# Kernel optimization log

Hardware: AMD Instinct MI355X
Metric: run time of the kernel (lower is better)

The kernel has to match this reference:

```python
import jax, jax.numpy as jnp
import numpy as np
from jax import lax

B, L, V, EMB = 256, 256, 14, 512
K = 16  # LSH bits (capped so 2**k fits int32)


def _conv2d(x, w, b):
    # x: [B,C,H,W], w: [O,I,3,3], padding=1 -> SAME
    y = lax.conv_general_dilated(x, w, (1, 1), ((1, 1), (1, 1)),
                                 dimension_numbers=("NCHW", "OIHW", "NCHW"))
    return y + b[None, :, None, None]


def _maxpool1d(x):  # [B,C,L] -> [B,C,L//2], kernel=stride=2
    b, c, l = x.shape
    return x.reshape(b, c, l // 2, 2).max(-1)


def _branch(tokens, emb, cw, cb, lw, lb):
    # Embedding -> pool over sequence -> Conv2d(3x3,pad1) on [C, L//2, 1] -> Linear
    e = emb[tokens]                     # [B,L,512]
    e = jnp.transpose(e, (0, 2, 1))     # [B,512,L]
    e = _maxpool1d(e)[..., None]        # [B,512,L//2,1]
    e = _conv2d(e, cw, cb)              # [B,256,L//2,1]
    return e.reshape(e.shape[0], -1) @ lw + lb


def _fog_of_war(enemy_out, rand_proj):
    # lsh_hash: random projection -> sign bits -> integer representation
    bits = (enemy_out @ rand_proj > 0).astype(jnp.int32)          # [B,K]
    pow2 = 2 ** jnp.arange(K - 1, -1, -1, dtype=jnp.int32)
    integer_repr = (bits * pow2).sum(axis=1)                      # [B] (computed as in original; loop doesn't read it)
    n = integer_repr.shape[0]
    # Greedy loop: remainder starts as arange(n); all counts are 1, so argmax
    # picks the first remaining index each iteration, which is then removed.
    def step(mask, _):
        idx = jnp.argmax(mask)  # first True = smallest remaining index
        return mask.at[idx].set(False), idx
    _, order = lax.scan(step, jnp.ones((n,), jnp.bool_), None, length=n)
    return order  # == arange(n), the original's deterministic result


def setup_inputs() -> dict:
    key = jax.random.key(0)
    ks = jax.random.split(key, 18)
    s = 0.02
    return {
        "x": jax.random.randint(ks[0], (B, L), 0, V, dtype=jnp.int32),
        "enemy_emb": jax.random.normal(ks[1], (V, EMB), jnp.float32) * s,
        "enemy_conv_w": jax.random.normal(ks[2], (256, 512, 3, 3), jnp.float32) * s,
        "enemy_conv_b": jax.random.normal(ks[3], (256,), jnp.float32) * s,
        "enemy_lin_w": jax.random.normal(ks[4], (256 * (L // 2), 128), jnp.float32) * s,
        "enemy_lin_b": jax.random.normal(ks[5], (128,), jnp.float32) * s,
        "rand_proj": jax.random.normal(ks[6], (128, K), jnp.float32),
        "manip_conv_w": jax.random.normal(ks[7], (64, 128, 3, 3), jnp.float32) * s,
        "manip_conv_b": jax.random.normal(ks[8], (64,), jnp.float32) * s,
        "manip_lin_w": jax.random.normal(ks[9], (64 * (L // 2), 256), jnp.float32) * s,
        "manip_lin_b": jax.random.normal(ks[10], (256,), jnp.float32) * s,
        "friend_emb": jax.random.normal(ks[11], (V, EMB), jnp.float32) * s,
        "friend_conv_w": jax.random.normal(ks[12], (256, 512, 3, 3), jnp.float32) * s,
        "friend_conv_b": jax.random.normal(ks[13], (256,), jnp.float32) * s,
        "friend_lin1_w": jax.random.normal(ks[14], (256 * (L // 2), 128), jnp.float32) * s,
        "friend_lin1_b": jax.random.normal(ks[15], (128,), jnp.float32) * s,
        "friend_lin2_w": jax.random.normal(ks[16], (128, V), jnp.float32) * s,
        "friend_lin2_b": jax.random.normal(ks[17], (V,), jnp.float32) * s,
    }


def reference(x, enemy_emb, enemy_conv_w, enemy_conv_b, enemy_lin_w, enemy_lin_b,
              rand_proj, manip_conv_w, manip_conv_b, manip_lin_w, manip_lin_b,
              friend_emb, friend_conv_w, friend_conv_b, friend_lin1_w, friend_lin1_b,
              friend_lin2_w, friend_lin2_b):
    # enemy branch
    enemy_out = jax.nn.softmax(
        _branch(x, enemy_emb, enemy_conv_w, enemy_conv_b, enemy_lin_w, enemy_lin_b), axis=1)  # [B,128]
    # fog_of_war: LSH hash + greedy set-cover loop -> index order
    perm = _fog_of_war(enemy_out, rand_proj)  # [B] int
    # probability manipulator: Conv2d(128,64) expects [B,128,L//2,1]
    m_in = jnp.broadcast_to(enemy_out[perm][:, :, None, None], (B, 128, L // 2, 1))
    m = jax.nn.relu(_conv2d(m_in, manip_conv_w, manip_conv_b))   # [B,64,L//2,1]
    m = m.reshape(B, -1) @ manip_lin_w + manip_lin_b             # [B,256]
    # friend branch consumes manipulator output as a token sequence (Embedding needs ints)
    tokens = (jnp.floor(jnp.abs(m) * 100.0) % V).astype(jnp.int32)  # [B,256]
    f = _branch(tokens, friend_emb, friend_conv_w, friend_conv_b, friend_lin1_w, friend_lin1_b)
    f = f @ friend_lin2_w + friend_lin2_b                        # [B,14]
    return jax.nn.softmax(f, axis=1)
```

## Files before the change

kernel.cpp:

```cpp
#include <hip/hip_runtime.h>
#include <hip/hip_bf16.h>
#include <math.h>

#define BB    256
#define LL    256
#define NV    14
#define EMBD  512
#define H2    128
#define OC    256
#define NP    196
#define JD    128
#define MO    64
#define MJ    256

#define CB_MAIN   294
#define CB_MANIPW 48
#define CB_LINT   32

using s16x8 = __attribute__((ext_vector_type(8))) short;
using f32x4 = __attribute__((ext_vector_type(4))) float;

static __device__ __forceinline__ unsigned pk2(float a, float b) {
    union { __hip_bfloat162 h; unsigned u; } c;
    c.h = __float22bfloat162_rn(make_float2(a, b));
    return c.u;
}
static __device__ __forceinline__ void hilo2(float y0, float y1,
                                             unsigned &hi, unsigned &lo) {
    hi = pk2(y0, y1);
    float h0 = __uint_as_float(hi << 16);
    float h1 = __uint_as_float(hi & 0xFFFF0000u);
    lo = pk2(y0 - h0, y1 - h1);
}

__global__ void k_prep(const float* __restrict__ cw_e, const float* __restrict__ cw_f,
                       float* __restrict__ cwT) {
    __shared__ float T[48][66];
    int bid = blockIdx.x;
    int t = threadIdx.x;
    int ic = bid & 31;
    int oc = (bid >> 5) & 3;
    int br = bid >> 7;
    int i0 = ic * 16, o0 = oc * 64;
    const float* cw = br ? cw_f : cw_e;
    int ol = t >> 2, part = t & 3;
    const float* src = cw + ((size_t)(o0 + ol) * EMBD + i0) * 9 + part * 36;
    #pragma unroll
    for (int ii = 0; ii < 4; ++ii)
        #pragma unroll
        for (int kh = 0; kh < 3; ++kh)
            T[kh * 16 + part * 4 + ii][ol] = src[ii * 9 + kh * 3 + 1];
    __syncthreads();
    int lane = t & 63, r0 = t >> 6;
    for (int rr = r0; rr < 48; rr += 4) {
        int kh = rr >> 4, il = rr & 15;
        cwT[(((size_t)(br * 3 + kh)) * EMBD + i0 + il) * OC + o0 + lane] = T[rr][lane];
    }
}

__global__ __launch_bounds__(512) void k_contrib(
        const float* __restrict__ emb_e, const float* __restrict__ emb_f,
        const float* __restrict__ cwT,
        const float* __restrict__ cb_e, const float* __restrict__ cb_f,
        const float* __restrict__ mcw, const float* __restrict__ mlw,
        float* __restrict__ C, float* __restrict__ Wc, float* __restrict__ Lint) {
    int bid = blockIdx.x;
    int t = threadIdx.x;
    if (bid < CB_MAIN) {
        int qg = bid % 49;
        int kh = (bid / 49) % 3;
        int br = bid / 147;
        int o = t & 255, ih = t >> 8;
        const float* emb = br ? emb_f : emb_e;

        __shared__ float Pl[4][512];
        __shared__ float Rd[4][2][256];
        for (int idx = t; idx < 4 * 512; idx += 512) {
            int row = idx >> 9, col = idx & 511;
            int q = qg * 4 + row;
            int t1 = q / NV, t2 = q % NV;
            Pl[row][col] = fmaxf(emb[t1 * EMBD + col], emb[t2 * EMBD + col]);
        }
        __syncthreads();

        const float* w = cwT + ((size_t)(br * 3 + kh) * EMBD + ih * 256) * OC + o;
        float acc[4] = {0.f, 0.f, 0.f, 0.f};
        #pragma unroll 8
        for (int i = 0; i < 256; i++) {
            float wv = w[(size_t)i * OC];
            #pragma unroll
            for (int qq = 0; qq < 4; qq++) acc[qq] = fmaf(wv, Pl[qq][ih * 256 + i], acc[qq]);
        }
        #pragma unroll
        for (int qq = 0; qq < 4; qq++) Rd[qq][ih][o] = acc[qq];
        __syncthreads();
        if (t < 256) {
            float cbv = (kh == 1) ? (br ? cb_f[o] : cb_e[o]) : 0.f;
            #pragma unroll
            for (int qq = 0; qq < 4; qq++)
                C[(((size_t)br * NP + qg * 4 + qq) * 3 + kh) * OC + o] =
                    Rd[qq][0][o] + Rd[qq][1][o] + cbv;
        }
    } else if (bid < CB_MAIN + CB_MANIPW) {
        int idx = (bid - CB_MAIN) * 512 + t;
        int o = idx & 63;
        int i = (idx >> 6) & 127;
        int cls = idx >> 13;
        const float* base = mcw + ((size_t)(o * 128 + i) * 3) * 3 + 1;
        float v = 0.f;
        if (cls != 2) { v += base[3]; v += base[6]; }
        else          { v += base[0]; v += base[3]; }
        if (cls == 1)   v += base[0];
        Wc[idx] = v;
    } else {
        int lb = bid - (CB_MAIN + CB_MANIPW);
        int o = lb * 2 + (t >> 8);
        int j = t & 255;
        float s = 0.f;
        for (int h = 1; h <= 126; h++)
            s += mlw[((size_t)(o * H2 + h)) * MJ + j];
        Lint[o * 256 + j] = s;
    }
}

template <int X3, int SK>
__global__ __launch_bounds__(512) void k_gemm(
        const int* __restrict__ tok, const float* __restrict__ C,
        const float* __restrict__ lw, float* __restrict__ partial) {
    __shared__ unsigned short Ah[2][64][SK + 4];
    __shared__ unsigned short Al[X3 ? 2 : 1][X3 ? 64 : 1][X3 ? SK + 4 : 1];
    __shared__ unsigned short Bh[2][128][SK + 4];
    __shared__ unsigned short Bl[X3 ? 2 : 1][X3 ? 128 : 1][X3 ? SK + 4 : 1];

    const int h  = blockIdx.x;
    const int B0 = blockIdx.y * 64;
    const int t  = threadIdx.x;
    constexpr int NST = 256 / SK;
    constexpr int KQ  = SK / 8;
    constexpr int KPT = SK / 16;

    const int am = t >> 3;
    const int kq = (t & 7) * KQ;
    const int* tb = tok + (size_t)(B0 + am) * LL;
    const int q1 = tb[2 * h] * NV + tb[2 * h + 1];
    const float* r1 = C + ((size_t)q1 * 3 + 1) * OC + kq;
    const float* r0 = nullptr;
    const float* r2 = nullptr;
    if (h > 0)      { int q0 = tb[2 * h - 2] * NV + tb[2 * h - 1]; r0 = C + ((size_t)q0 * 3 + 0) * OC + kq; }
    if (h < H2 - 1) { int q2 = tb[2 * h + 2] * NV + tb[2 * h + 3]; r2 = C + ((size_t)q2 * 3 + 2) * OC + kq; }

    const int j0b = (t & 31) * 4;
    const int k0  = (t >> 5) * KPT;
    const float* wsrc = lw + (((size_t)k0 * H2) + h) * JD + j0b;

    float4 ya[SK / 32], yb[SK / 32], yc[SK / 32], wv4[KPT];

    auto load = [&](int s) {
        #pragma unroll
        for (int p = 0; p < SK / 32; ++p) {
            ya[p] = *(const float4*)(r1 + s * SK + 4 * p);
            if (r0) yb[p] = *(const float4*)(r0 + s * SK + 4 * p);
            else    yb[p] = make_float4(0, 0, 0, 0);
            if (r2) yc[p] = *(const float4*)(r2 + s * SK + 4 * p);
            else    yc[p] = make_float4(0, 0, 0, 0);
        }
        #pragma unroll
        for (int kk = 0; kk < KPT; ++kk)
            wv4[kk] = *(const float4*)(wsrc + ((size_t)(s * SK) + kk) * (H2 * JD));
    };

    auto store = [&](int buf) {
        #pragma unroll
        for (int p = 0; p < SK / 32; ++p) {
            float y[4];
            y[0] = ya[p].x + yb[p].x + yc[p].x; y[1] = ya[p].y + yb[p].y + yc[p].y;
            y[2] = ya[p].z + yb[p].z + yc[p].z; y[3] = ya[p].w + yb[p].w + yc[p].w;
            if (X3) {
                unsigned h0, h1, l0, l1;
                hilo2(y[0], y[1], h0, l0);
                hilo2(y[2], y[3], h1, l1);
                *(uint2*)&Ah[buf][am][kq + 4 * p] = make_uint2(h0, h1);
                *(uint2*)&Al[buf][am][kq + 4 * p] = make_uint2(l0, l1);
            } else {
                *(uint2*)&Ah[buf][am][kq + 4 * p] =
                    make_uint2(pk2(y[0], y[1]), pk2(y[2], y[3]));
            }
        }
        #pragma unroll
        for (int jj = 0; jj < 4; ++jj) {
            float wf[KPT];
            #pragma unroll
            for (int kk = 0; kk < KPT; ++kk)
                wf[kk] = ((const float*)&wv4[kk])[jj];
            if constexpr (KPT == 2) {
                if (X3) {
                    unsigned hu, lu;
                    hilo2(wf[0], wf[1], hu, lu);
                    *(unsigned*)&Bh[buf][j0b + jj][k0] = hu;
                    *(unsigned*)&Bl[buf][j0b + jj][k0] = lu;
                } else {
                    *(unsigned*)&Bh[buf][j0b + jj][k0] = pk2(wf[0], wf[1]);
                }
            } else {
                if (X3) {
                    unsigned h0, h1, l0, l1;
                    hilo2(wf[0], wf[1], h0, l0);
                    hilo2(wf[2], wf[3], h1, l1);
                    *(uint2*)&Bh[buf][j0b + jj][k0] = make_uint2(h0, h1);
                    *(uint2*)&Bl[buf][j0b + jj][k0] = make_uint2(l0, l1);
                } else {
                    *(uint2*)&Bh[buf][j0b + jj][k0] =
                        make_uint2(pk2(wf[0], wf[1]), pk2(wf[2], wf[3]));
                }
            }
        }
    };

    const int lane = t & 63, wid = t >> 6;
    const int Wm = (wid >> 2) * 32;
    const int Wn = (wid & 3) * 32;
    const int fr = lane & 15;
    const int g8 = (lane >> 4) * 8;

    f32x4 acc[2][2] = {};

    auto rd8 = [&](const unsigned short* p) -> s16x8 {
        union { s16x8 v; uint2 u[2]; } tmp;
        tmp.u[0] = *(const uint2*)(p);
        tmp.u[1] = *(const uint2*)(p + 4);
        return tmp.v;
    };

    auto compute = [&](int buf) {
        #pragma unroll
        for (int kk0 = 0; kk0 < SK; kk0 += 32) {
            s16x8 a_h[2], b_h[2];
            #pragma unroll
            for (int mf = 0; mf < 2; ++mf) a_h[mf] = rd8(&Ah[buf][Wm + mf * 16 + fr][kk0 + g8]);
            #pragma unroll
            for (int nf = 0; nf < 2; ++nf) b_h[nf] = rd8(&Bh[buf][Wn + nf * 16 + fr][kk0 + g8]);
            #pragma unroll
            for (int mf = 0; mf < 2; ++mf)
                #pragma unroll
                for (int nf = 0; nf < 2; ++nf)
                    acc[mf][nf] = __builtin_amdgcn_mfma_f32_16x16x32_bf16(a_h[mf], b_h[nf], acc[mf][nf], 0, 0, 0);
            if (X3) {
                s16x8 a_l[2], b_l[2];
                #pragma unroll
                for (int mf = 0; mf < 2; ++mf) a_l[mf] = rd8(&Al[buf][Wm + mf * 16 + fr][kk0 + g8]);
                #pragma unroll
                for (int nf = 0; nf < 2; ++nf) b_l[nf] = rd8(&Bl[buf][Wn + nf * 16 + fr][kk0 + g8]);
                #pragma unroll
                for (int mf = 0; mf < 2; ++mf)
                    #pragma unroll
                    for (int nf = 0; nf < 2; ++nf) {
                        acc[mf][nf] = __builtin_amdgcn_mfma_f32_16x16x32_bf16(a_h[mf], b_l[nf], acc[mf][nf], 0, 0, 0);
                        acc[mf][nf] = __builtin_amdgcn_mfma_f32_16x16x32_bf16(a_l[mf], b_h[nf], acc[mf][nf], 0, 0, 0);
                    }
            }
        }
    };

    load(0);
    store(0);
    __syncthreads();
    for (int s = 0; s < NST; ++s) {
        if (s < NST - 1) load(s + 1);
        compute(s & 1);
        if (s < NST - 1) store((s + 1) & 1);
        __syncthreads();
    }

    float* pb = partial + (((size_t)(B0 + Wm)) * H2 + h) * JD + Wn;
    #pragma unroll
    for (int mf = 0; mf < 2; ++mf)
        #pragma unroll
        for (int nf = 0; nf < 2; ++nf)
            #pragma unroll
            for (int r = 0; r < 4; ++r) {
                int row = mf * 16 + (lane >> 4) * 4 + r;
                int col = nf * 16 + fr;
                pb[(size_t)row * H2 * JD + col] = acc[mf][nf][r];
            }
}

__global__ __launch_bounds__(512) void k_fuseE(
        const float* __restrict__ partial, const float* __restrict__ elb,
        const float* __restrict__ Wc, const float* __restrict__ mcb,
        const float* __restrict__ mlw, const float* __restrict__ Lint,
        const float* __restrict__ mlb, int* __restrict__ tokens) {
    int b = blockIdx.x, t = threadIdx.x;
    __shared__ float S[4][128];
    __shared__ float eo[128];
    __shared__ float m3[3][64];
    __shared__ float red[128];
    __shared__ float mt[2][256];

    int j = t & 127, hh = t >> 7;
    float s = 0.f;
    const float* pbase = partial + (size_t)b * H2 * JD + j;
    for (int h = hh * 32; h < hh * 32 + 32; ++h)
        s += pbase[(size_t)h * JD];
    S[hh][j] = s;
    __syncthreads();
    if (t < 128) {
        float v = (S[0][t] + S[1][t]) + (S[2][t] + S[3][t]) + elb[t];
        S[0][t] = v;
        red[t] = v;
    }
    __syncthreads();
    for (int st = 64; st > 0; st >>= 1) {
        if (t < st) red[t] = fmaxf(red[t], red[t + st]);
        __syncthreads();
    }
    float mx = red[0];
    __syncthreads();
    if (t < 128) {
        float e = expf(S[0][t] - mx);
        eo[t] = e;
        red[t] = e;
    }
    __syncthreads();
    for (int st = 64; st > 0; st >>= 1) {
        if (t < st) red[t] += red[t + st];
        __syncthreads();
    }
    float inv = 1.f / red[0];
    __syncthreads();
    if (t < 128) eo[t] *= inv;
    __syncthreads();
    if (t < 192) {
        int cls = t >> 6, o = t & 63;
        float a = mcb[o];
        const float* wp = Wc + (size_t)cls * 128 * 64 + o;
        for (int i = 0; i < 128; ++i) a = fmaf(eo[i], wp[(size_t)i * 64], a);
        m3[cls][o] = fmaxf(a, 0.f);
    }
    __syncthreads();
    {
        int ihh = t >> 8, jj = t & 255;
        float a = ihh ? 0.f : mlb[jj];
        for (int o = ihh * 32; o < ihh * 32 + 32; ++o) {
            a = fmaf(m3[0][o], mlw[((size_t)(o * H2 + 0)) * MJ + jj], a);
            a = fmaf(m3[1][o], Lint[(size_t)o * MJ + jj], a);
            a = fmaf(m3[2][o], mlw[((size_t)(o * H2 + 127)) * MJ + jj], a);
        }
        mt[ihh][jj] = a;
    }
    __syncthreads();
    if (t < 256) {
        float a = mt[0][t] + mt[1][t];
        tokens[(size_t)b * LL + t] = ((int)floorf(fabsf(a) * 100.f)) % NV;
    }
}

__global__ __launch_bounds__(512) void k_fuseF(
        const float* __restrict__ partial, const float* __restrict__ flb1,
        const float* __restrict__ fl2, const float* __restrict__ fb2,
        float* __restrict__ outp) {
    int b = blockIdx.x, t = threadIdx.x;
    __shared__ float S[4][128];
    __shared__ float f1[128];
    __shared__ float sl[NV];
    int j = t & 127, hh = t >> 7;
    float s = 0.f;
    const float* pbase = partial + (size_t)b * H2 * JD + j;
    for (int h = hh * 32; h < hh * 32 + 32; ++h)
        s += pbase[(size_t)h * JD];
    S[hh][j] = s;
    __syncthreads();
    if (t < 128) f1[t] = (S[0][t] + S[1][t]) + (S[2][t] + S[3][t]) + flb1[t];
    __syncthreads();
    if (t < NV) {
        float a = fb2[t];
        for (int jj = 0; jj < 128; ++jj) a = fmaf(f1[jj], fl2[(size_t)jj * NV + t], a);
        sl[t] = a;
    }
    __syncthreads();
    if (t < NV) {
        float mx = -1e30f;
        for (int u = 0; u < NV; ++u) mx = fmaxf(mx, sl[u]);
        float ss = 0.f;
        for (int u = 0; u < NV; ++u) ss += expf(sl[u] - mx);
        outp[(size_t)b * NV + t] = expf(sl[t] - mx) / ss;
    }
}

extern "C" void kernel_launch(void* const* d_in, const int* in_sizes, int n_in,
                              void* d_out, int out_size, void* d_ws, size_t ws_size,
                              hipStream_t stream) {
    const int*   x    = (const int*)d_in[0];
    const float* eemb = (const float*)d_in[1];
    const float* ecw  = (const float*)d_in[2];
    const float* ecb  = (const float*)d_in[3];
    const float* elw  = (const float*)d_in[4];
    const float* elb  = (const float*)d_in[5];
    const float* mcw  = (const float*)d_in[7];
    const float* mcb  = (const float*)d_in[8];
    const float* mlw  = (const float*)d_in[9];
    const float* mlb  = (const float*)d_in[10];
    const float* femb = (const float*)d_in[11];
    const float* fcw  = (const float*)d_in[12];
    const float* fcb  = (const float*)d_in[13];
    const float* flw1 = (const float*)d_in[14];
    const float* flb1 = (const float*)d_in[15];
    const float* fl2  = (const float*)d_in[16];
    const float* fb2  = (const float*)d_in[17];
    float* outp = (float*)d_out;

    char* w = (char*)d_ws;
    size_t off = 0;
    auto alloc = [&](size_t bytes) {
        void* p = w + off;
        off = (off + bytes + 255) & ~(size_t)255;
        return p;
    };
    float* cwT    = (float*)alloc(2ull * 3 * EMBD * OC * 4);
    float* C      = (float*)alloc(2ull * NP * 3 * OC * 4);
    float* Wc     = (float*)alloc(3ull * 128 * 64 * 4);
    float* Lint   = (float*)alloc(64ull * MJ * 4);
    int*   tokens = (int*)alloc((size_t)BB * LL * 4);
    float* partial= (float*)alloc((size_t)BB * H2 * JD * 4);

    const float* C_e = C;
    const float* C_f = C + (size_t)NP * 3 * OC;

    k_prep<<<256, 256, 0, stream>>>(ecw, fcw, cwT);
    k_contrib<<<CB_MAIN + CB_MANIPW + CB_LINT, 512, 0, stream>>>(
        eemb, femb, cwT, ecb, fcb, mcw, mlw, C, Wc, Lint);

    k_gemm<1, 32><<<dim3(H2, 4), 512, 0, stream>>>(x, C_e, elw, partial);
    k_fuseE<<<BB, 512, 0, stream>>>(partial, elb, Wc, mcb, mlw, Lint, mlb, tokens);

    k_gemm<0, 64><<<dim3(H2, 4), 512, 0, stream>>>(tokens, C_f, flw1, partial);
    k_fuseF<<<BB, 512, 0, stream>>>(partial, flb1, fl2, fb2, outp);
}
```

Baseline: 75.10 us.

## Retile per-position GEMM to 32-row blocks covering two sequence positions each

The per-position GEMM kernel now gives each block 32 batch rows instead of 64 and has it loop over two adjacent sequence positions, accumulating both into one partial result. The partial buffer is halved and the fuse kernels reduce over 64 position groups instead of 128. This halves the partial-sum traffic and the reduction work, keeping the block count at 512. In exchange each block runs twice as many pipeline stages with fewer MFMAs per wave per stage, so the weight tile loaded per stage is reused by half as many rows.

New measurement: 84.99 us. +13.2%, slower.

```diff
diff --git a/kernel.cpp b/kernel.cpp
--- a/kernel.cpp
+++ b/kernel.cpp
@@ -12,6 +12,7 @@
 #define JD    128
 #define MO    64
 #define MJ    256
+#define GH    64
 
 #define CB_MAIN   294
 #define CB_MANIPW 48
@@ -124,66 +125,93 @@
 }
 
 template <int X3, int SK>
-__global__ __launch_bounds__(512) void k_gemm(
+__global__ __launch_bounds__(512) void k_gemm32(
         const int* __restrict__ tok, const float* __restrict__ C,
         const float* __restrict__ lw, float* __restrict__ partial) {
-    __shared__ unsigned short Ah[2][64][SK + 4];
-    __shared__ unsigned short Al[X3 ? 2 : 1][X3 ? 64 : 1][X3 ? SK + 4 : 1];
+    constexpr int NST = 256 / SK;
+    constexpr int U   = 2 * NST;
+    constexpr int KA  = SK / 16;
+    constexpr int KPT = SK / 16;
+
+    __shared__ unsigned short Ah[2][32][SK + 4];
+    __shared__ unsigned short Al[X3 ? 2 : 1][X3 ? 32 : 1][X3 ? SK + 4 : 1];
     __shared__ unsigned short Bh[2][128][SK + 4];
     __shared__ unsigned short Bl[X3 ? 2 : 1][X3 ? 128 : 1][X3 ? SK + 4 : 1];
 
-    const int h  = blockIdx.x;
-    const int B0 = blockIdx.y * 64;
+    const int hg = blockIdx.x;
+    const int h0 = hg * 2;
+    const int B0 = blockIdx.y * 32;
     const int t  = threadIdx.x;
-    constexpr int NST = 256 / SK;
-    constexpr int KQ  = SK / 8;
-    constexpr int KPT = SK / 16;
-
-    const int am = t >> 3;
-    const int kq = (t & 7) * KQ;
+
+    const int am = t >> 4;
+    const int kq = (t & 15) * KA;
     const int* tb = tok + (size_t)(B0 + am) * LL;
-    const int q1 = tb[2 * h] * NV + tb[2 * h + 1];
-    const float* r1 = C + ((size_t)q1 * 3 + 1) * OC + kq;
-    const float* r0 = nullptr;
-    const float* r2 = nullptr;
-    if (h > 0)      { int q0 = tb[2 * h - 2] * NV + tb[2 * h - 1]; r0 = C + ((size_t)q0 * 3 + 0) * OC + kq; }
-    if (h < H2 - 1) { int q2 = tb[2 * h + 2] * NV + tb[2 * h + 3]; r2 = C + ((size_t)q2 * 3 + 2) * OC + kq; }
 
     const int j0b = (t & 31) * 4;
     const int k0  = (t >> 5) * KPT;
-    const float* wsrc = lw + (((size_t)k0 * H2) + h) * JD + j0b;
-
-    float4 ya[SK / 32], yb[SK / 32], yc[SK / 32], wv4[KPT];
+
+    const float *r1, *r0, *r2, *wsrc;
+    auto setptr = [&](int h) {
+        int q1 = tb[2 * h] * NV + tb[2 * h + 1];
+        r1 = C + ((size_t)q1 * 3 + 1) * OC + kq;
+        r0 = nullptr; r2 = nullptr;
+        if (h > 0)      { int q0 = tb[2 * h - 2] * NV + tb[2 * h - 1]; r0 = C + ((size_t)q0 * 3 + 0) * OC + kq; }
+        if (h < H2 - 1) { int q2 = tb[2 * h + 2] * NV + tb[2 * h + 3]; r2 = C + ((size_t)q2 * 3 + 2) * OC + kq; }
+        wsrc = lw + ((size_t)k0 * H2 + h) * JD + j0b;
+    };
+
+    float ya[KA], ybv[KA], ycv[KA];
+    float4 wv4[KPT];
+
+    auto ldv = [&](const float* p, float* d) {
+        if constexpr (KA == 2) {
+            float2 v = *(const float2*)p;
+            d[0] = v.x; d[1] = v.y;
+        } else {
+            float4 v = *(const float4*)p;
+            d[0] = v.x; d[1] = v.y; d[2] = v.z; d[3] = v.w;
+        }
+    };
 
     auto load = [&](int s) {
-        #pragma unroll
-        for (int p = 0; p < SK / 32; ++p) {
-            ya[p] = *(const float4*)(r1 + s * SK + 4 * p);
-            if (r0) yb[p] = *(const float4*)(r0 + s * SK + 4 * p);
-            else    yb[p] = make_float4(0, 0, 0, 0);
-            if (r2) yc[p] = *(const float4*)(r2 + s * SK + 4 * p);
-            else    yc[p] = make_float4(0, 0, 0, 0);
+        ldv(r1 + s * SK, ya);
+        if (r0) {
+            ldv(r0 + s * SK, ybv);
+        } else {
+            for (int e = 0; e < KA; ++e) ybv[e] = 0.f;
+        }
+        if (r2) {
+            ldv(r2 + s * SK, ycv);
+        } else {
+            for (int e = 0; e < KA; ++e) ycv[e] = 0.f;
         }
         #pragma unroll
         for (int kk = 0; kk < KPT; ++kk)
-            wv4[kk] = *(const float4*)(wsrc + ((size_t)(s * SK) + kk) * (H2 * JD));
+            wv4[kk] = *(const float4*)(wsrc + ((size_t)(s * SK + kk) * H2) * JD);
     };
 
     auto store = [&](int buf) {
-        #pragma unroll
-        for (int p = 0; p < SK / 32; ++p) {
-            float y[4];
-            y[0] = ya[p].x + yb[p].x + yc[p].x; y[1] = ya[p].y + yb[p].y + yc[p].y;
-            y[2] = ya[p].z + yb[p].z + yc[p].z; y[3] = ya[p].w + yb[p].w + yc[p].w;
+        float y[KA];
+        #pragma unroll
+        for (int e = 0; e < KA; ++e) y[e] = ya[e] + ybv[e] + ycv[e];
+        if constexpr (KA == 2) {
             if (X3) {
-                unsigned h0, h1, l0, l1;
-                hilo2(y[0], y[1], h0, l0);
-                hilo2(y[2], y[3], h1, l1);
-                *(uint2*)&Ah[buf][am][kq + 4 * p] = make_uint2(h0, h1);
-                *(uint2*)&Al[buf][am][kq + 4 * p] = make_uint2(l0, l1);
+                unsigned hu, lu;
+                hilo2(y[0], y[1], hu, lu);
+                *(unsigned*)&Ah[buf][am][kq] = hu;
+                *(unsigned*)&Al[buf][am][kq] = lu;
             } else {
-                *(uint2*)&Ah[buf][am][kq + 4 * p] =
-                    make_uint2(pk2(y[0], y[1]), pk2(y[2], y[3]));
+                *(unsigned*)&Ah[buf][am][kq] = pk2(y[0], y[1]);
+            }
+        } else {
+            if (X3) {
+                unsigned h0u, h1u, l0u, l1u;
+                hilo2(y[0], y[1], h0u, l0u);
+                hilo2(y[2], y[3], h1u, l1u);
+                *(uint2*)&Ah[buf][am][kq] = make_uint2(h0u, h1u);
+                *(uint2*)&Al[buf][am][kq] = make_uint2(l0u, l1u);
+            } else {
+                *(uint2*)&Ah[buf][am][kq] = make_uint2(pk2(y[0], y[1]), pk2(y[2], y[3]));
             }
         }
         #pragma unroll
@@ -203,11 +231,11 @@
                 }
             } else {
                 if (X3) {
-                    unsigned h0, h1, l0, l1;
-                    hilo2(wf[0], wf[1], h0, l0);
-                    hilo2(wf[2], wf[3], h1, l1);
-                    *(uint2*)&Bh[buf][j0b + jj][k0] = make_uint2(h0, h1);
-                    *(uint2*)&Bl[buf][j0b + jj][k0] = make_uint2(l0, l1);
+                    unsigned h0u, h1u, l0u, l1u;
+                    hilo2(wf[0], wf[1], h0u, l0u);
+                    hilo2(wf[2], wf[3], h1u, l1u);
+                    *(uint2*)&Bh[buf][j0b + jj][k0] = make_uint2(h0u, h1u);
+                    *(uint2*)&Bl[buf][j0b + jj][k0] = make_uint2(l0u, l1u);
                 } else {
                     *(uint2*)&Bh[buf][j0b + jj][k0] =
                         make_uint2(pk2(wf[0], wf[1]), pk2(wf[2], wf[3]));
@@ -217,12 +245,12 @@
     };
 
     const int lane = t & 63, wid = t >> 6;
-    const int Wm = (wid >> 2) * 32;
+    const int Wm = (wid >> 2) * 16;
     const int Wn = (wid & 3) * 32;
     const int fr = lane & 15;
     const int g8 = (lane >> 4) * 8;
 
-    f32x4 acc[2][2] = {};
+    f32x4 acc[2] = {};
 
     auto rd8 = [&](const unsigned short* p) -> s16x8 {
         union { s16x8 v; uint2 u[2]; } tmp;
@@ -234,54 +262,52 @@
     auto compute = [&](int buf) {
         #pragma unroll
         for (int kk0 = 0; kk0 < SK; kk0 += 32) {
-            s16x8 a_h[2], b_h[2];
-            #pragma unroll
-            for (int mf = 0; mf < 2; ++mf) a_h[mf] = rd8(&Ah[buf][Wm + mf * 16 + fr][kk0 + g8]);
+            s16x8 a_h = rd8(&Ah[buf][Wm + fr][kk0 + g8]);
+            s16x8 b_h[2];
             #pragma unroll
             for (int nf = 0; nf < 2; ++nf) b_h[nf] = rd8(&Bh[buf][Wn + nf * 16 + fr][kk0 + g8]);
             #pragma unroll
-            for (int mf = 0; mf < 2; ++mf)
-                #pragma unroll
-                for (int nf = 0; nf < 2; ++nf)
-                    acc[mf][nf] = __builtin_amdgcn_mfma_f32_16x16x32_bf16(a_h[mf], b_h[nf], acc[mf][nf], 0, 0, 0);
+            for (int nf = 0; nf < 2; ++nf)
+                acc[nf] = __builtin_amdgcn_mfma_f32_16x16x32_bf16(a_h, b_h[nf], acc[nf], 0, 0, 0);
             if (X3) {
-                s16x8 a_l[2], b_l[2];
-                #pragma unroll
-                for (int mf = 0; mf < 2; ++mf) a_l[mf] = rd8(&Al[buf][Wm + mf * 16 + fr][kk0 + g8]);
+                s16x8 a_l = rd8(&Al[buf][Wm + fr][kk0 + g8]);
+                s16x8 b_l[2];
                 #pragma unroll
                 for (int nf = 0; nf < 2; ++nf) b_l[nf] = rd8(&Bl[buf][Wn + nf * 16 + fr][kk0 + g8]);
                 #pragma unroll
-                for (int mf = 0; mf < 2; ++mf)
-                    #pragma unroll
-                    for (int nf = 0; nf < 2; ++nf) {
-                        acc[mf][nf] = __builtin_amdgcn_mfma_f32_16x16x32_bf16(a_h[mf], b_l[nf], acc[mf][nf], 0, 0, 0);
-                        acc[mf][nf] = __builtin_amdgcn_mfma_f32_16x16x32_bf16(a_l[mf], b_h[nf], acc[mf][nf], 0, 0, 0);
-                    }
+                for (int nf = 0; nf < 2; ++nf) {
+                    acc[nf] = __builtin_amdgcn_mfma_f32_16x16x32_bf16(a_h, b_l[nf], acc[nf], 0, 0, 0);
+                    acc[nf] = __builtin_amdgcn_mfma_f32_16x16x32_bf16(a_l, b_h[nf], acc[nf], 0, 0, 0);
+                }
             }
         }
     };
 
+    setptr(h0);
     load(0);
     store(0);
     __syncthreads();
-    for (int s = 0; s < NST; ++s) {
-        if (s < NST - 1) load(s + 1);
-        compute(s & 1);
-        if (s < NST - 1) store((s + 1) & 1);
+    int cur = 0;
+    for (int u = 0; u < U; ++u) {
+        int un = u + 1;
+        if (un < U) {
+            if (un == NST) setptr(h0 + 1);
+            load(un % NST);
+        }
+        compute(cur);
+        if (un < U) store(cur ^ 1);
         __syncthreads();
-    }
-
-    float* pb = partial + (((size_t)(B0 + Wm)) * H2 + h) * JD + Wn;
+        cur ^= 1;
+    }
+
+    float* pb = partial + (((size_t)(B0 + Wm)) * GH + hg) * JD + Wn;
     #pragma unroll
-    for (int mf = 0; mf < 2; ++mf)
-        #pragma unroll
-        for (int nf = 0; nf < 2; ++nf)
-            #pragma unroll
-            for (int r = 0; r < 4; ++r) {
-                int row = mf * 16 + (lane >> 4) * 4 + r;
-                int col = nf * 16 + fr;
-                pb[(size_t)row * H2 * JD + col] = acc[mf][nf][r];
-            }
+    for (int nf = 0; nf < 2; ++nf)
+        #pragma unroll
+        for (int r = 0; r < 4; ++r) {
+            int row = (lane >> 4) * 4 + r;
+            pb[(size_t)row * GH * JD + nf * 16 + fr] = acc[nf][r];
+        }
 }
 
 __global__ __launch_bounds__(512) void k_fuseE(
@@ -298,8 +324,8 @@
 
     int j = t & 127, hh = t >> 7;
     float s = 0.f;
-    const float* pbase = partial + (size_t)b * H2 * JD + j;
-    for (int h = hh * 32; h < hh * 32 + 32; ++h)
+    const float* pbase = partial + (size_t)b * GH * JD + j;
+    for (int h = hh * 16; h < hh * 16 + 16; ++h)
         s += pbase[(size_t)h * JD];
     S[hh][j] = s;
     __syncthreads();
@@ -364,8 +390,8 @@
     __shared__ float sl[NV];
     int j = t & 127, hh = t >> 7;
     float s = 0.f;
-    const float* pbase = partial + (size_t)b * H2 * JD + j;
-    for (int h = hh * 32; h < hh * 32 + 32; ++h)
+    const float* pbase = partial + (size_t)b * GH * JD + j;
+    for (int h = hh * 16; h < hh * 16 + 16; ++h)
         s += pbase[(size_t)h * JD];
     S[hh][j] = s;
     __syncthreads();
@@ -420,7 +446,7 @@
     float* Wc     = (float*)alloc(3ull * 128 * 64 * 4);
     float* Lint   = (float*)alloc(64ull * MJ * 4);
     int*   tokens = (int*)alloc((size_t)BB * LL * 4);
-    float* partial= (float*)alloc((size_t)BB * H2 * JD * 4);
+    float* partial= (float*)alloc((size_t)BB * GH * JD * 4);
 
     const float* C_e = C;
     const float* C_f = C + (size_t)NP * 3 * OC;
@@ -429,9 +455,9 @@
     k_contrib<<<CB_MAIN + CB_MANIPW + CB_LINT, 512, 0, stream>>>(
         eemb, femb, cwT, ecb, fcb, mcw, mlw, C, Wc, Lint);
 
-    k_gemm<1, 32><<<dim3(H2, 4), 512, 0, stream>>>(x, C_e, elw, partial);
+    k_gemm32<1, 32><<<dim3(GH, 8), 512, 0, stream>>>(x, C_e, elw, partial);
     k_fuseE<<<BB, 512, 0, stream>>>(partial, elb, Wc, mcb, mlw, Lint, mlb, tokens);
 
-    k_gemm<0, 64><<<dim3(H2, 4), 512, 0, stream>>>(tokens, C_f, flw1, partial);
+    k_gemm32<0, 64><<<dim3(GH, 8), 512, 0, stream>>>(tokens, C_f, flw1, partial);
     k_fuseF<<<BB, 512, 0, stream>>>(partial, flb1, fl2, fb2, outp);
 }
```
